# Optimization experiments

Measured on AMD Instinct MI355X. Metric: run time of the kernel, lower is better.

## Reference

```python
import jax, jax.numpy as jnp
import numpy as np

H = 1024
I = 4096
E = 8
B, S, K = 2, 2048, 2


def setup_inputs() -> dict:
    key = jax.random.key(0)
    k1, k2, k3, k4, k5, k6 = jax.random.split(key, 6)
    x = jax.random.normal(k1, (B, S, H), dtype=jnp.float32)
    expert_indices = jax.random.randint(k2, (B, S, K), 0, E, dtype=jnp.int32)
    expert_weights = jax.random.uniform(k3, (B, S, K), dtype=jnp.float32)
    gate_proj = jax.random.normal(k4, (E, I, H), dtype=jnp.float32) * 0.02
    up_proj = jax.random.normal(k5, (E, I, H), dtype=jnp.float32) * 0.02
    down_proj = jax.random.normal(k6, (E, H, I), dtype=jnp.float32) * 0.02
    return {"x": x, "expert_indices": expert_indices, "expert_weights": expert_weights,
            "gate_proj": gate_proj, "up_proj": up_proj, "down_proj": down_proj}


def reference(x, expert_indices, expert_weights, gate_proj, up_proj, down_proj):
    b, s, h = x.shape
    e = gate_proj.shape[0]
    k = expert_indices.shape[-1]
    xf = x.reshape(-1, h)                       # [N, H]
    idx = expert_indices.reshape(-1, k)         # [N, K]
    wts = expert_weights.reshape(-1, k)         # [N, K]
    # combine[n, e] = sum over slots k with idx[n,k]==e of wts[n,k]
    onehot = jax.nn.one_hot(idx, e, dtype=x.dtype)            # [N, K, E]
    combine = jnp.einsum('nk,nke->ne', wts, onehot)           # [N, E]
    out = jnp.zeros_like(xf)
    # Fixed small unrolled loop over experts (data dims fully vectorized).
    for ei in range(e):
        gate = jax.nn.silu(xf @ gate_proj[ei].T)              # [N, I]
        up = xf @ up_proj[ei].T                               # [N, I]
        out = out + ((gate * up) @ down_proj[ei].T) * combine[:, ei:ei + 1]
    return out.reshape(b, s, h)
```

## Files before the change

kernel.cpp:

```cpp
#include <hip/hip_runtime.h>
#include <hip/hip_bf16.h>
#include <cstdint>

#define HD 1024
#define ID 4096
#define NE 8
#define NTOK 4096
#define NASS 8192
#define NWL 72

typedef unsigned short u16;
typedef __attribute__((ext_vector_type(8))) __bf16 bf16x8;
typedef __attribute__((ext_vector_type(4))) float f32x4;

__device__ __forceinline__ void async16(void* lds, const void* g) {
  __builtin_amdgcn_global_load_lds(
      (const __attribute__((address_space(1))) uint32_t*)g,
      (__attribute__((address_space(3))) uint32_t*)lds, 16, 0, 0);
}

__device__ __forceinline__ u16 f2b(float f) {
  __bf16 h = (__bf16)f;
  return __builtin_bit_cast(u16, h);
}

__device__ __forceinline__ bf16x8 cvt8(const float* p) {
  const float4* q = (const float4*)p;
  float4 a = q[0], b = q[1];
  bf16x8 v;
  v[0] = (__bf16)a.x; v[1] = (__bf16)a.y; v[2] = (__bf16)a.z; v[3] = (__bf16)a.w;
  v[4] = (__bf16)b.x; v[5] = (__bf16)b.y; v[6] = (__bf16)b.z; v[7] = (__bf16)b.w;
  return v;
}

__global__ void k_pre(const float* __restrict__ x, const float* __restrict__ gate,
                      const float* __restrict__ up, u16* __restrict__ xb,
                      u16* __restrict__ wg, u16* __restrict__ wu,
                      float* __restrict__ out) {
  const size_t stride = (size_t)gridDim.x * 256;
  for (size_t v = (size_t)blockIdx.x * 256 + threadIdx.x; v < 8912896ull; v += stride) {
    const float* src; u16* dst; size_t off;
    if (v < 524288ull)        { src = x;    dst = xb; off = v;
      float4 z = {0.f, 0.f, 0.f, 0.f};
      float4* op = (float4*)(out + off * 8);
      op[0] = z; op[1] = z;
    }
    else if (v < 4718592ull)  { src = gate; dst = wg; off = v - 524288ull; }
    else                      { src = up;   dst = wu; off = v - 4718592ull; }
    size_t i8 = off * 8;
    *(bf16x8*)(dst + i8) = cvt8(src + i8);
  }
}

__global__ void k_meta(const int* __restrict__ eidx, int* __restrict__ offsets,
                       int* __restrict__ wl, int* __restrict__ tokl) {
  __shared__ int cnt[NE], offs_s[NE + 1], cur[NE];
  int t = threadIdx.x;
  if (t < NE) cnt[t] = 0;
  __syncthreads();
  for (int i = t; i < NASS; i += 1024) atomicAdd(&cnt[eidx[i]], 1);
  __syncthreads();
  if (t == 0) {
    int s = 0;
    for (int e = 0; e < NE; ++e) { offs_s[e] = s; s += cnt[e]; }
    offs_s[NE] = s;
    int w = 0;
    for (int e = 0; e < NE; ++e)
      for (int mt = 0; mt * 128 < cnt[e]; ++mt) wl[w++] = (e << 16) | mt;
    for (; w < NWL; ++w) wl[w] = -1;
  }
  if (t < NE) cur[t] = 0;
  __syncthreads();
  for (int i = t; i < NASS; i += 1024) {
    int e = eidx[i];
    int p = atomicAdd(&cur[e], 1);
    tokl[offs_s[e] + p] = i;
  }
  if (t <= NE) offsets[t] = offs_s[t];
}

__global__ __launch_bounds__(256, 2) void k_g1(
    const u16* __restrict__ xb, const u16* __restrict__ wg, const u16* __restrict__ wu,
    const float* __restrict__ down, u16* __restrict__ wd,
    const int* __restrict__ offsets, const int* __restrict__ wl,
    const int* __restrict__ tokl, u16* __restrict__ interm) {
  const int bx = blockIdx.x;
  const int t = threadIdx.x;
  if (bx >= 32) {
    int cid = (bx - 32) + 32 * (int)blockIdx.y;
    if (cid < 2048) {
#pragma unroll
      for (int l = 0; l < 8; ++l) {
        size_t i8 = (((size_t)cid * 8 + l) * 256 + t) * 8;
        *(bf16x8*)(wd + i8) = cvt8(down + i8);
      }
    }
    return;
  }
  const int wle = wl[blockIdx.y];
  if (wle < 0) return;
  const int e = wle >> 16;
  const int m0 = (wle & 0xffff) << 7;
  const int offs = offsets[e];
  const int Me = offsets[e + 1] - offs;
  const int n0 = bx * 128;
  const int lane = t & 63, wv = t >> 6;
  const int wm = wv & 1, wn = wv >> 1;

  __shared__ __align__(16) u16 As[128 * 64];
  __shared__ __align__(16) u16 Bg[128 * 64];
  __shared__ __align__(16) u16 Bu[128 * 64];

  const u16* asrc[4];
#pragma unroll
  for (int p = 0; p < 4; ++p) {
    int c = p * 256 + t;
    int r = c >> 3, c8 = c & 7;
    int row = m0 + r; if (row > Me - 1) row = Me - 1;
    asrc[p] = xb + (size_t)(tokl[offs + row] >> 1) * HD + c8 * 8;
  }
  const u16 *bgsrc[4], *busrc[4];
#pragma unroll
  for (int p = 0; p < 4; ++p) {
    int c = p * 256 + t;
    int r = c >> 3, c8 = c & 7;
    size_t boff = ((size_t)e * ID + n0 + r) * HD + c8 * 8;
    bgsrc[p] = wg + boff;
    busrc[p] = wu + boff;
  }

  f32x4 accg[4][4], accu[4][4];
#pragma unroll
  for (int mi = 0; mi < 4; ++mi)
#pragma unroll
    for (int ni = 0; ni < 4; ++ni) {
      accg[mi][ni] = (f32x4){0.f, 0.f, 0.f, 0.f};
      accu[mi][ni] = (f32x4){0.f, 0.f, 0.f, 0.f};
    }

  const int lrow = lane & 15, lk = (lane >> 4) * 8;
#pragma unroll 1
  for (int ks = 0; ks < HD / 64; ++ks) {
    __syncthreads();
#pragma unroll
    for (int p = 0; p < 4; ++p) {
      async16((char*)As + (p * 256 + wv * 64) * 16, asrc[p]);
      async16((char*)Bg + (p * 256 + wv * 64) * 16, bgsrc[p]);
      async16((char*)Bu + (p * 256 + wv * 64) * 16, busrc[p]);
    }
    __syncthreads();
#pragma unroll
    for (int kk = 0; kk < 2; ++kk) {
      bf16x8 af[4], bg[4], bu[4];
#pragma unroll
      for (int mi = 0; mi < 4; ++mi)
        af[mi] = *(const bf16x8*)&As[(wm * 64 + mi * 16 + lrow) * 64 + kk * 32 + lk];
#pragma unroll
      for (int ni = 0; ni < 4; ++ni) {
        bg[ni] = *(const bf16x8*)&Bg[(wn * 64 + ni * 16 + lrow) * 64 + kk * 32 + lk];
        bu[ni] = *(const bf16x8*)&Bu[(wn * 64 + ni * 16 + lrow) * 64 + kk * 32 + lk];
      }
#pragma unroll
      for (int mi = 0; mi < 4; ++mi)
#pragma unroll
        for (int ni = 0; ni < 4; ++ni) {
          accg[mi][ni] = __builtin_amdgcn_mfma_f32_16x16x32_bf16(af[mi], bg[ni], accg[mi][ni], 0, 0, 0);
          accu[mi][ni] = __builtin_amdgcn_mfma_f32_16x16x32_bf16(af[mi], bu[ni], accu[mi][ni], 0, 0, 0);
        }
    }
#pragma unroll
    for (int p = 0; p < 4; ++p) { asrc[p] += 64; bgsrc[p] += 64; busrc[p] += 64; }
  }

#pragma unroll
  for (int mi = 0; mi < 4; ++mi) {
    int rb = wm * 64 + mi * 16 + (lane >> 4) * 4;
#pragma unroll
    for (int ni = 0; ni < 4; ++ni) {
      int col = n0 + wn * 64 + ni * 16 + (lane & 15);
#pragma unroll
      for (int j = 0; j < 4; ++j) {
        int row = m0 + rb + j;
        if (row < Me) {
          float g = accg[mi][ni][j], u = accu[mi][ni][j];
          float s = g / (1.f + __expf(-g));
          interm[(size_t)(offs + row) * ID + col] = f2b(s * u);
        }
      }
    }
  }
}

__global__ __launch_bounds__(256, 2) void k_g2(
    const u16* __restrict__ interm, const u16* __restrict__ wd,
    const int* __restrict__ offsets, const int* __restrict__ wl,
    const int* __restrict__ tokl, const float* __restrict__ ewt,
    float* __restrict__ out) {
  const int wle = wl[blockIdx.y];
  if (wle < 0) return;
  const int e = wle >> 16;
  const int m0 = (wle & 0xffff) << 7;
  const int offs = offsets[e];
  const int Me = offsets[e + 1] - offs;
  const int n0 = blockIdx.x * 256;
  const int t = threadIdx.x, lane = t & 63, wv = t >> 6;
  const int wm = wv & 1, wn = wv >> 1;

  __shared__ __align__(16) u16 As[128 * 64];
  __shared__ __align__(16) u16 Bs[256 * 64];

  const u16* asrc[4];
#pragma unroll
  for (int p = 0; p < 4; ++p) {
    int c = p * 256 + t;
    int r = c >> 3, c8 = c & 7;
    int row = m0 + r; if (row > Me - 1) row = Me - 1;
    asrc[p] = interm + (size_t)(offs + row) * ID + c8 * 8;
  }
  const u16* bsrc[8];
#pragma unroll
  for (int p = 0; p < 8; ++p) {
    int c = p * 256 + t;
    int r = c >> 3, c8 = c & 7;
    bsrc[p] = wd + ((size_t)e * HD + n0 + r) * ID + c8 * 8;
  }

  f32x4 acc[4][8];
#pragma unroll
  for (int mi = 0; mi < 4; ++mi)
#pragma unroll
    for (int ni = 0; ni < 8; ++ni) acc[mi][ni] = (f32x4){0.f, 0.f, 0.f, 0.f};

  const int lrow = lane & 15, lk = (lane >> 4) * 8;
#pragma unroll 1
  for (int ks = 0; ks < ID / 64; ++ks) {
    __syncthreads();
#pragma unroll
    for (int p = 0; p < 4; ++p)
      async16((char*)As + (p * 256 + wv * 64) * 16, asrc[p]);
#pragma unroll
    for (int p = 0; p < 8; ++p)
      async16((char*)Bs + (p * 256 + wv * 64) * 16, bsrc[p]);
    __syncthreads();
#pragma unroll
    for (int kk = 0; kk < 2; ++kk) {
      bf16x8 af[4], bfr[8];
#pragma unroll
      for (int mi = 0; mi < 4; ++mi)
        af[mi] = *(const bf16x8*)&As[(wm * 64 + mi * 16 + lrow) * 64 + kk * 32 + lk];
#pragma unroll
      for (int ni = 0; ni < 8; ++ni)
        bfr[ni] = *(const bf16x8*)&Bs[(wn * 128 + ni * 16 + lrow) * 64 + kk * 32 + lk];
#pragma unroll
      for (int mi = 0; mi < 4; ++mi)
#pragma unroll
        for (int ni = 0; ni < 8; ++ni)
          acc[mi][ni] = __builtin_amdgcn_mfma_f32_16x16x32_bf16(af[mi], bfr[ni], acc[mi][ni], 0, 0, 0);
    }
#pragma unroll
    for (int p = 0; p < 4; ++p) asrc[p] += 64;
#pragma unroll
    for (int p = 0; p < 8; ++p) bsrc[p] += 64;
  }

#pragma unroll
  for (int mi = 0; mi < 4; ++mi) {
    int rb = wm * 64 + mi * 16 + (lane >> 4) * 4;
#pragma unroll
    for (int j = 0; j < 4; ++j) {
      int row = m0 + rb + j;
      if (row < Me) {
        int aid = tokl[offs + row];
        float w = ewt[aid];
        float* orow = out + (size_t)(aid >> 1) * HD;
#pragma unroll
        for (int ni = 0; ni < 8; ++ni) {
          int col = n0 + wn * 128 + ni * 16 + (lane & 15);
          atomicAdd(orow + col, w * acc[mi][ni][j]);
        }
      }
    }
  }
}

extern "C" void kernel_launch(void* const* d_in, const int* in_sizes, int n_in,
                              void* d_out, int out_size, void* d_ws, size_t ws_size,
                              hipStream_t stream) {
  const float* x    = (const float*)d_in[0];
  const int*   eidx = (const int*)d_in[1];
  const float* ewt  = (const float*)d_in[2];
  const float* gate = (const float*)d_in[3];
  const float* up   = (const float*)d_in[4];
  const float* down = (const float*)d_in[5];
  float* out = (float*)d_out;
  char* ws = (char*)d_ws;

  constexpr size_t OFF_INTERM = 0;
  constexpr size_t OFF_XB     = 67108864;
  constexpr size_t OFF_META   = 75497472;
  constexpr size_t OFF_TOK    = 75498496;
  constexpr size_t OFF_WD     = 75531264;
  constexpr size_t OFF_WG     = 142640128;
  constexpr size_t OFF_WU     = 209748992;

  u16* interm  = (u16*)(ws + OFF_INTERM);
  u16* xb      = (u16*)(ws + OFF_XB);
  int* offsets = (int*)(ws + OFF_META);
  int* wl      = (int*)(ws + OFF_META + 64);
  int* tokl    = (int*)(ws + OFF_TOK);
  u16* wd      = (u16*)(ws + OFF_WD);
  u16* wg      = (u16*)(ws + OFF_WG);
  u16* wu      = (u16*)(ws + OFF_WU);

  k_pre<<<dim3(2048), dim3(256), 0, stream>>>(x, gate, up, xb, wg, wu, out);
  k_meta<<<dim3(1), dim3(1024), 0, stream>>>(eidx, offsets, wl, tokl);
  k_g1<<<dim3(64, NWL), dim3(256), 0, stream>>>(xb, wg, wu, down, wd, offsets, wl, tokl, interm);
  k_g2<<<dim3(HD / 256, NWL), dim3(256), 0, stream>>>(interm, wd, offsets, wl, tokl, ewt, out);
}
```

Before: 465.4 us.

## Double-buffer gate/up GEMM LDS tiles with BK=32 async prefetch

Splits the gate/up GEMM K-loop into 32-wide steps with two LDS buffers. The next tile's global-to-LDS async loads are issued before the MFMAs on the current buffer, so loads overlap with compute and one barrier per step is removed. In exchange, each K-step is half as deep, so barriers and address setup per unit of MFMA work go up. The loads are not explicitly waited on before the barrier, so correctness depends on the barrier draining the outstanding async loads.

```diff
diff --git a/kernel.cpp b/kernel.cpp
--- a/kernel.cpp
+++ b/kernel.cpp
@@ -107,26 +107,35 @@
   const int lane = t & 63, wv = t >> 6;
   const int wm = wv & 1, wn = wv >> 1;
 
-  __shared__ __align__(16) u16 As[128 * 64];
-  __shared__ __align__(16) u16 Bg[128 * 64];
-  __shared__ __align__(16) u16 Bu[128 * 64];
-
-  const u16* asrc[4];
-#pragma unroll
-  for (int p = 0; p < 4; ++p) {
+  __shared__ __align__(16) u16 As[2][128 * 32];
+  __shared__ __align__(16) u16 Bg[2][128 * 32];
+  __shared__ __align__(16) u16 Bu[2][128 * 32];
+
+  const u16* asrc[2];
+#pragma unroll
+  for (int p = 0; p < 2; ++p) {
     int c = p * 256 + t;
-    int r = c >> 3, c8 = c & 7;
+    int r = c >> 2, c8 = (c & 3) * 8;
     int row = m0 + r; if (row > Me - 1) row = Me - 1;
-    asrc[p] = xb + (size_t)(tokl[offs + row] >> 1) * HD + c8 * 8;
-  }
-  const u16 *bgsrc[4], *busrc[4];
-#pragma unroll
-  for (int p = 0; p < 4; ++p) {
+    asrc[p] = xb + (size_t)(tokl[offs + row] >> 1) * HD + c8;
+  }
+  const u16 *bgsrc[2], *busrc[2];
+#pragma unroll
+  for (int p = 0; p < 2; ++p) {
     int c = p * 256 + t;
-    int r = c >> 3, c8 = c & 7;
-    size_t boff = ((size_t)e * ID + n0 + r) * HD + c8 * 8;
+    int r = c >> 2, c8 = (c & 3) * 8;
+    size_t boff = ((size_t)e * ID + n0 + r) * HD + c8;
     bgsrc[p] = wg + boff;
     busrc[p] = wu + boff;
+  }
+
+#define STAGE1(b, ks)                                                           \
+  {                                                                             \
+    _Pragma("unroll") for (int p = 0; p < 2; ++p) {                             \
+      async16((char*)As[b] + (p * 256 + wv * 64) * 16, asrc[p] + (ks) * 32);    \
+      async16((char*)Bg[b] + (p * 256 + wv * 64) * 16, bgsrc[p] + (ks) * 32);   \
+      async16((char*)Bu[b] + (p * 256 + wv * 64) * 16, busrc[p] + (ks) * 32);   \
+    }                                                                           \
   }
 
   f32x4 accg[4][4], accu[4][4];
@@ -138,39 +147,33 @@
       accu[mi][ni] = (f32x4){0.f, 0.f, 0.f, 0.f};
     }
 
+  STAGE1(0, 0);
+  __syncthreads();
+
   const int lrow = lane & 15, lk = (lane >> 4) * 8;
 #pragma unroll 1
-  for (int ks = 0; ks < HD / 64; ++ks) {
+  for (int ks = 0; ks < HD / 32; ++ks) {
+    const int curb = ks & 1;
+    if (ks < HD / 32 - 1) STAGE1(curb ^ 1, ks + 1);
+    bf16x8 af[4], bg[4], bu[4];
+#pragma unroll
+    for (int mi = 0; mi < 4; ++mi)
+      af[mi] = *(const bf16x8*)&As[curb][(wm * 64 + mi * 16 + lrow) * 32 + lk];
+#pragma unroll
+    for (int ni = 0; ni < 4; ++ni) {
+      bg[ni] = *(const bf16x8*)&Bg[curb][(wn * 64 + ni * 16 + lrow) * 32 + lk];
+      bu[ni] = *(const bf16x8*)&Bu[curb][(wn * 64 + ni * 16 + lrow) * 32 + lk];
+    }
+#pragma unroll
+    for (int mi = 0; mi < 4; ++mi)
+#pragma unroll
+      for (int ni = 0; ni < 4; ++ni) {
+        accg[mi][ni] = __builtin_amdgcn_mfma_f32_16x16x32_bf16(af[mi], bg[ni], accg[mi][ni], 0, 0, 0);
+        accu[mi][ni] = __builtin_amdgcn_mfma_f32_16x16x32_bf16(af[mi], bu[ni], accu[mi][ni], 0, 0, 0);
+      }
     __syncthreads();
-#pragma unroll
-    for (int p = 0; p < 4; ++p) {
-      async16((char*)As + (p * 256 + wv * 64) * 16, asrc[p]);
-      async16((char*)Bg + (p * 256 + wv * 64) * 16, bgsrc[p]);
-      async16((char*)Bu + (p * 256 + wv * 64) * 16, busrc[p]);
-    }
-    __syncthreads();
-#pragma unroll
-    for (int kk = 0; kk < 2; ++kk) {
-      bf16x8 af[4], bg[4], bu[4];
-#pragma unroll
-      for (int mi = 0; mi < 4; ++mi)
-        af[mi] = *(const bf16x8*)&As[(wm * 64 + mi * 16 + lrow) * 64 + kk * 32 + lk];
-#pragma unroll
-      for (int ni = 0; ni < 4; ++ni) {
-        bg[ni] = *(const bf16x8*)&Bg[(wn * 64 + ni * 16 + lrow) * 64 + kk * 32 + lk];
-        bu[ni] = *(const bf16x8*)&Bu[(wn * 64 + ni * 16 + lrow) * 64 + kk * 32 + lk];
-      }
-#pragma unroll
-      for (int mi = 0; mi < 4; ++mi)
-#pragma unroll
-        for (int ni = 0; ni < 4; ++ni) {
-          accg[mi][ni] = __builtin_amdgcn_mfma_f32_16x16x32_bf16(af[mi], bg[ni], accg[mi][ni], 0, 0, 0);
-          accu[mi][ni] = __builtin_amdgcn_mfma_f32_16x16x32_bf16(af[mi], bu[ni], accu[mi][ni], 0, 0, 0);
-        }
-    }
-#pragma unroll
-    for (int p = 0; p < 4; ++p) { asrc[p] += 64; bgsrc[p] += 64; busrc[p] += 64; }
-  }
+  }
+#undef STAGE1
 
 #pragma unroll
   for (int mi = 0; mi < 4; ++mi) {
```

After: 460.5 us. About the same (-1.1%).
